# Kernel optimization log

Measured on AMD Instinct MI355X. Metric: run time of the kernel, lower is better.

## Reference

```python
import jax, jax.numpy as jnp
import numpy as np

B, C, L = 4, 512, 4096
H = 8
DH = C // H
MLP = 2048


def _ln(x, g, b, eps=1e-5):
    mu = x.mean(-1, keepdims=True)
    var = ((x - mu) ** 2).mean(-1, keepdims=True)
    return (x - mu) / jnp.sqrt(var + eps) * g + b


def setup_inputs() -> dict:
    key = jax.random.key(0)
    ks = jax.random.split(key, 16)
    s = 0.02
    d = {
        "x": jax.random.normal(ks[0], (B, C, L), jnp.float32),
        "Wq": jax.random.normal(ks[1], (C, C), jnp.float32) * s,
        "bq": jnp.zeros((C,), jnp.float32),
        "gq": jnp.ones((C,), jnp.float32),
        "betaq": jnp.zeros((C,), jnp.float32),
        "Wk": jax.random.normal(ks[2], (C, C), jnp.float32) * s,
        "bk": jnp.zeros((C,), jnp.float32),
        "gk": jnp.ones((C,), jnp.float32),
        "betak": jnp.zeros((C,), jnp.float32),
        "Wv": jax.random.normal(ks[3], (C, C), jnp.float32) * s,
        "bv": jnp.zeros((C,), jnp.float32),
        "gv": jnp.ones((C,), jnp.float32),
        "betav": jnp.zeros((C,), jnp.float32),
        "Wkq": jax.random.normal(ks[4], (C, C), jnp.float32) * s,
        "bkq": jnp.zeros((C,), jnp.float32),
        "Wkk": jax.random.normal(ks[5], (C, C), jnp.float32) * s,
        "bkk": jnp.zeros((C,), jnp.float32),
        "g_attn": jnp.ones((C,), jnp.float32),
        "b_attn": jnp.zeros((C,), jnp.float32),
        "W1": jax.random.normal(ks[6], (C, MLP), jnp.float32) * s,
        "b1": jnp.zeros((MLP,), jnp.float32),
        "W2": jax.random.normal(ks[7], (MLP, C), jnp.float32) * s,
        "b2": jnp.zeros((C,), jnp.float32),
    }
    return d


def _split_heads(t):
    # [B, L, C] -> [B, H, L, DH]
    b, l, _ = t.shape
    return t.reshape(b, l, H, DH).transpose(0, 2, 1, 3)


def reference(x, Wq, bq, gq, betaq, Wk, bk, gk, betak, Wv, bv, gv, betav,
              Wkq, bkq, Wkk, bkk, g_attn, b_attn, W1, b1, W2, b2):
    # x: [B, C, L] -> flatten(2).permute(0,2,1) -> [B, L, C]
    xf = jnp.transpose(x, (0, 2, 1))
    Q = _ln(xf @ Wq + bq, gq, betaq)            # [B, L, C]
    K = _ln(xf @ Wk + bk, gk, betak)            # [B, L, C]
    V = _ln(xf @ Wv + bv, gv, betav)            # [B, L, C]
    # add zero token to K, V (seq dim)
    z = jnp.zeros((x.shape[0], 1, C), x.dtype)
    K = jnp.concatenate([z, K], axis=1)         # [B, Lk, C], Lk = L+1
    V = jnp.concatenate([z, V], axis=1)
    phiQ = jnp.tanh(Q @ Wkq + bkq) + 1.0        # [B, L, C]
    phiK = jnp.tanh(K @ Wkk + bkk) + 1.0        # [B, Lk, C]

    Qh, Kh, Vh = _split_heads(Q), _split_heads(K), _split_heads(V)
    pQ, pK = _split_heads(phiQ), _split_heads(phiK)  # [B,H,L,DH], [B,H,Lk,DH]

    # softmax-reweighted phi_K: score from mean-query probe against K
    q_probe = Qh.mean(axis=2)                                   # [B,H,DH]
    score = jnp.einsum('bhd,bhld->bhl', q_probe, Kh) / jnp.sqrt(jnp.float32(DH))
    score = jax.nn.softmax(score, axis=-1)                      # [B,H,Lk]
    pKw = pK * score[..., None]                                 # [B,H,Lk,DH]

    kv = jnp.einsum('bhld,bhle->bhde', pKw, Vh)                 # [B,H,DH,DH]
    num = jnp.einsum('bhqd,bhde->bhqe', pQ, kv)                 # [B,H,L,DH]
    ksum = pKw.sum(axis=2)                                      # [B,H,DH]
    bottom = jnp.einsum('bhqd,bhd->bhq', pQ, ksum)[..., None] + 1e-6
    out_h = num / bottom                                        # [B,H,L,DH]

    out = out_h.transpose(0, 2, 1, 3).reshape(x.shape[0], -1, C)  # [B,L,C]
    a = _ln(out, g_attn, b_attn)
    m = jax.nn.gelu(a @ W1 + b1, approximate=False) @ W2 + b2
    res = a + m                                                 # residual MLP
    res = jnp.transpose(res, (0, 2, 1))                         # [B,C,L]
    return res + x
```

## Files before the change

### kernel.cpp

```cpp
#include <hip/hip_runtime.h>
#include <math.h>

#define B_ 4
#define C_ 512
#define L_ 4096
#define H_ 8
#define DH_ 64
#define MLP_ 2048
#define BL_ (B_*L_)
#define LK_ (L_+1)

typedef _Float16 f16;
typedef _Float16 f16x8 __attribute__((ext_vector_type(8)));
typedef _Float16 f16x4 __attribute__((ext_vector_type(4)));
typedef float f32x4 __attribute__((ext_vector_type(4)));

__device__ __forceinline__ void gl16(void* lds, const void* g) {
  __builtin_amdgcn_global_load_lds((const __attribute__((address_space(1))) void*)g,
                                   (__attribute__((address_space(3))) void*)lds,
                                   16, 0, 0);
}

__device__ __forceinline__ float frcp(float x) { return __builtin_amdgcn_rcpf(x); }

__global__ __launch_bounds__(256) void transpose_w5(const float* __restrict__ Wq,
                                                    const float* __restrict__ Wk,
                                                    const float* __restrict__ Wv,
                                                    const float* __restrict__ Wkq,
                                                    const float* __restrict__ Wkk,
                                                    f16* __restrict__ dst) {
  int z = blockIdx.z;
  const float* W = (z == 0) ? Wq : (z == 1) ? Wk : (z == 2) ? Wv : (z == 3) ? Wkq : Wkk;
  f16* Wt = dst + (size_t)z * C_ * C_;
  __shared__ float tile[32][33];
  int n0 = blockIdx.x * 32, k0 = blockIdx.y * 32;
  int tx = threadIdx.x & 31, ty = threadIdx.x >> 5;
#pragma unroll
  for (int i = 0; i < 4; ++i)
    tile[ty + i * 8][tx] = W[(size_t)(k0 + ty + i * 8) * C_ + n0 + tx];
  __syncthreads();
#pragma unroll
  for (int i = 0; i < 4; ++i)
    Wt[(size_t)(n0 + ty + i * 8) * C_ + k0 + tx] = (f16)tile[tx][ty + i * 8];
}

__global__ __launch_bounds__(256) void transpose_w(const float* __restrict__ W,
                                                   f16* __restrict__ Wt, int K, int N) {
  __shared__ float tile[32][33];
  int n0 = blockIdx.x * 32, k0 = blockIdx.y * 32;
  int tx = threadIdx.x & 31, ty = threadIdx.x >> 5;
#pragma unroll
  for (int i = 0; i < 4; ++i)
    tile[ty + i * 8][tx] = W[(size_t)(k0 + ty + i * 8) * N + n0 + tx];
  __syncthreads();
#pragma unroll
  for (int i = 0; i < 4; ++i)
    Wt[(size_t)(n0 + ty + i * 8) * K + k0 + tx] = (f16)tile[tx][ty + i * 8];
}

__global__ __launch_bounds__(256) void transpose_x(const float* __restrict__ x,
                                                   f16* __restrict__ xf) {
  __shared__ float tile[32][33];
  int b = blockIdx.z;
  int l0 = blockIdx.x * 32, c0 = blockIdx.y * 32;
  int tx = threadIdx.x & 31, ty = threadIdx.x >> 5;
#pragma unroll
  for (int i = 0; i < 4; ++i)
    tile[ty + i * 8][tx] = x[((size_t)b * C_ + c0 + ty + i * 8) * L_ + l0 + tx];
  __syncthreads();
#pragma unroll
  for (int i = 0; i < 4; ++i)
    xf[((size_t)b * L_ + l0 + ty + i * 8) * C_ + c0 + tx] = (f16)tile[tx][ty + i * 8];
}

__global__ __launch_bounds__(256) void pack_params(
    const float* bq, const float* bk, const float* bv,
    const float* gq, const float* gk, const float* gv,
    const float* betaq, const float* betak, const float* betav,
    const float* bkq, const float* bkk,
    float* bqkv, float* gqkv, float* betaqkv, float* bphi) {
  int i = blockIdx.x * 256 + threadIdx.x;
  int w = i >> 9, c = i & 511;
  bqkv[i]    = (w == 0 ? bq : (w == 1 ? bk : bv))[c];
  gqkv[i]    = (w == 0 ? gq : (w == 1 ? gk : gv))[c];
  betaqkv[i] = (w == 0 ? betaq : (w == 1 ? betak : betav))[c];
  if (i < 1024) bphi[i] = (i < 512) ? bkq[i] : bkk[i - 512];
}

template <int EPI>
__global__ __launch_bounds__(256, 2) void gemm64(const f16* __restrict__ A,
                                                 const f16* __restrict__ Bt,
                                                 const float* __restrict__ bias,
                                                 f16* __restrict__ Ch,
                                                 int N, int K,
                                                 const float* __restrict__ Bot,
                                                 const f16* __restrict__ Ares,
                                                 const float* __restrict__ Xres,
                                                 float* __restrict__ Fout,
                                                 long long zA, long long zB,
                                                 long long zC, long long zBias,
                                                 long long zBot) {
  __shared__ f16 smem[2 * 128 * 128];
  A  += (size_t)blockIdx.z * zA;
  Bt += (size_t)blockIdx.z * zB;
  if (EPI != 6) Ch += (size_t)blockIdx.z * zC;
  if (EPI == 3) Bot += (size_t)blockIdx.z * zBot;
  else          bias += (size_t)blockIdx.z * zBias;

  const int tid = threadIdx.x;
  const int lane = tid & 63, wv = tid >> 6;
  const int wm = wv >> 1, wn = wv & 1;
  const int bm = blockIdx.x * 128, bn = blockIdx.y * 128;
  const int l15 = lane & 15, q = lane >> 4;

  const int srow = tid >> 3;
  const int schunk = (tid & 7) ^ (srow & 7);
  const f16* pa = A + (size_t)(bm + srow) * K + schunk * 8;
  const f16* pb = Bt + (size_t)(bn + srow) * K + schunk * 8;
  f16* la = smem + tid * 8;
  f16* lb = smem + 8192 + tid * 8;
  const int sw0 = (q ^ (lane & 7)) * 8;
  const int sw1 = ((4 + q) ^ (lane & 7)) * 8;

  f32x4 acc[4][4] = {};

#pragma unroll
  for (int p = 0; p < 4; ++p) gl16(la + p * 2048, pa + (size_t)p * 32 * K);
#pragma unroll
  for (int p = 0; p < 4; ++p) gl16(lb + p * 2048, pb + (size_t)p * 32 * K);

  int cur = 0;
  for (int k0 = 0; k0 < K; k0 += 64) {
    __syncthreads();
    const int nxt = cur ^ 1;
    if (k0 + 64 < K) {
#pragma unroll
      for (int p = 0; p < 4; ++p) gl16(la + nxt * 16384 + p * 2048, pa + (size_t)p * 32 * K + k0 + 64);
#pragma unroll
      for (int p = 0; p < 4; ++p) gl16(lb + nxt * 16384 + p * 2048, pb + (size_t)p * 32 * K + k0 + 64);
    }
    const f16* As = smem + cur * 16384;
    const f16* Bs = As + 8192;
#pragma unroll
    for (int ks = 0; ks < 2; ++ks) {
      const int sw = ks ? sw1 : sw0;
      f16x8 af[4], bf[4];
#pragma unroll
      for (int i = 0; i < 4; ++i)
        af[i] = *(const f16x8*)&As[(wm * 64 + i * 16 + l15) * 64 + sw];
#pragma unroll
      for (int j = 0; j < 4; ++j)
        bf[j] = *(const f16x8*)&Bs[(wn * 64 + j * 16 + l15) * 64 + sw];
#pragma unroll
      for (int i = 0; i < 4; ++i)
#pragma unroll
        for (int j = 0; j < 4; ++j)
          acc[i][j] = __builtin_amdgcn_mfma_f32_16x16x32_f16(af[i], bf[j], acc[i][j], 0, 0, 0);
    }
    cur = nxt;
  }

  __syncthreads();
#pragma unroll
  for (int j = 0; j < 4; ++j) {
    int lc = wn * 64 + j * 16 + l15;
    float bb = (EPI == 3) ? 0.f : bias[bn + lc];
#pragma unroll
    for (int i = 0; i < 4; ++i) {
#pragma unroll
      for (int r = 0; r < 4; ++r) {
        int lr = wm * 64 + i * 16 + q * 4 + r;
        float v = acc[i][j][r] + bb;
        if (EPI == 1) {
          v = 2.0f * frcp(1.0f + __expf(-2.0f * v));
        } else if (EPI == 2) {
          v = v * frcp(1.0f + __expf(-1.5957691f * (v + 0.044715f * v * v * v)));
        } else if (EPI == 3) {
          v = v * frcp(Bot[(size_t)(bm + lr) * H_ + ((bn + lc) >> 6)] + 1e-6f);
        }
        smem[lr * 128 + ((((lc >> 3) ^ (lr & 15)) << 3) | (lc & 7))] = (f16)v;
      }
    }
  }
  __syncthreads();

  if (EPI != 6) {
#pragma unroll
    for (int p = 0; p < 8; ++p) {
      int idx = p * 256 + tid;
      int row = idx >> 4, ch = idx & 15;
      f16x8 vv = *(const f16x8*)&smem[row * 128 + ((ch ^ (row & 15)) << 3)];
      *(f16x8*)&Ch[(size_t)(bm + row) * N + bn + ch * 8] = vv;
    }
  } else {
#pragma unroll
    for (int p = 0; p < 8; ++p) {
      int idx = p * 256 + tid;
      int row = idx >> 4, ch = idx & 15;
      f16x8 av = *(const f16x8*)&Ares[(size_t)(bm + row) * C_ + bn + ch * 8];
      f16* sp = &smem[row * 128 + ((ch ^ (row & 15)) << 3)];
      f16x8 sv = *(const f16x8*)sp;
#pragma unroll
      for (int jj = 0; jj < 8; ++jj) sv[jj] = (f16)((float)sv[jj] + (float)av[jj]);
      *(f16x8*)sp = sv;
    }
    __syncthreads();
    int c = tid & 127, lh = tid >> 7;
    int b = bm >> 12, lbase = (bm & 4095) + lh * 64;
    const float* xp = Xres + ((size_t)b * C_ + bn + c) * L_ + lbase;
    float* op = Fout + ((size_t)b * C_ + bn + c) * L_ + lbase;
    int chi = c >> 3, clo = c & 7;
#pragma unroll
    for (int s = 0; s < 16; ++s) {
      int l = lh * 64 + s * 4;
      float4 xv = *(const float4*)(xp + s * 4);
      float4 r;
      r.x = (float)smem[(l + 0) * 128 + (((chi ^ ((l + 0) & 15)) << 3) | clo)] + xv.x;
      r.y = (float)smem[(l + 1) * 128 + (((chi ^ ((l + 1) & 15)) << 3) | clo)] + xv.y;
      r.z = (float)smem[(l + 2) * 128 + (((chi ^ ((l + 2) & 15)) << 3) | clo)] + xv.z;
      r.w = (float)smem[(l + 3) * 128 + (((chi ^ ((l + 3) & 15)) << 3) | clo)] + xv.w;
      *(float4*)(op + s * 4) = r;
    }
  }
}

__global__ __launch_bounds__(256) void ln16(const f16* __restrict__ X,
                                            const float* __restrict__ g,
                                            const float* __restrict__ bta,
                                            f16* __restrict__ Y, int threeway) {
  int wv = threadIdx.x >> 6, lane = threadIdx.x & 63;
  int r = blockIdx.x * 4 + wv;
  int token = r, which = 0;
  if (threeway) { token = r / 3; which = r - token * 3; }
  const f16* xr = X + (size_t)r * C_;
  f16x8 v = *(const f16x8*)(xr + lane * 8);
  float vals[8];
  float s = 0.f, s2 = 0.f;
#pragma unroll
  for (int j = 0; j < 8; ++j) { vals[j] = (float)v[j]; s += vals[j]; s2 += vals[j] * vals[j]; }
#pragma unroll
  for (int m_ = 1; m_ < 64; m_ <<= 1) { s += __shfl_xor(s, m_); s2 += __shfl_xor(s2, m_); }
  float mu = s * (1.f / C_);
  float var = s2 * (1.f / C_) - mu * mu;
  float rstd = rsqrtf(var + 1e-5f);
  const float* gp = g + which * C_;
  const float* bp = bta + which * C_;
  f16x8 o;
#pragma unroll
  for (int j = 0; j < 8; ++j) {
    int c = lane * 8 + j;
    o[j] = (f16)((vals[j] - mu) * rstd * gp[c] + bp[c]);
  }
  *(f16x8*)(Y + ((size_t)which * BL_ + token) * C_ + lane * 8) = o;
}

__global__ __launch_bounds__(256) void qprobe2(const f16* __restrict__ Q,
                                               float* __restrict__ qp) {
  int blk = blockIdx.x;
  int b = blk >> 6;
  int r0 = blk * 64;
  int t = threadIdx.x;
  int c8 = (t & 63) * 8, rg = t >> 6;
  float s[8] = {0.f, 0.f, 0.f, 0.f, 0.f, 0.f, 0.f, 0.f};
#pragma unroll
  for (int i = 0; i < 16; ++i) {
    const f16* row = Q + ((size_t)r0 + rg + i * 4) * C_ + c8;
    f16x8 v = *(const f16x8*)row;
#pragma unroll
    for (int j = 0; j < 8; ++j) s[j] += (float)v[j];
  }
  __shared__ float red[4][520];
#pragma unroll
  for (int j = 0; j < 8; ++j) red[rg][c8 + j] = s[j];
  __syncthreads();
  int c = t * 2;
  float a0 = red[0][c] + red[1][c] + red[2][c] + red[3][c];
  float a1 = red[0][c + 1] + red[1][c + 1] + red[2][c + 1] + red[3][c + 1];
  atomicAdd(&qp[b * C_ + c], a0);
  atomicAdd(&qp[b * C_ + c + 1], a1);
}

__global__ __launch_bounds__(256) void logits_kernel(const f16* __restrict__ Kh,
                                                     const float* __restrict__ qp,
                                                     float* __restrict__ score) {
  int wv = threadIdx.x >> 6, lane = threadIdx.x & 63;
  int token = blockIdx.x * 4 + wv;
  int b = token >> 12;
  int l = token & (L_ - 1);
  const f16* row = Kh + (size_t)token * C_;
  int h = lane >> 3, j0 = (lane & 7) * 8;
  const float* qph = qp + b * C_ + h * DH_ + j0;
  float p = 0.f;
#pragma unroll
  for (int j = 0; j < 8; ++j) p += qph[j] * (float)row[h * DH_ + j0 + j];
  p += __shfl_xor(p, 1); p += __shfl_xor(p, 2); p += __shfl_xor(p, 4);
  if ((lane & 7) == 0)
    score[((size_t)b * H_ + h) * LK_ + 1 + l] = p * (1.f / L_) * 0.125f;
}

__global__ __launch_bounds__(256) void softmax_kernel(float* __restrict__ score) {
  int bh = blockIdx.x, t = threadIdx.x;
  float* s = score + (size_t)bh * LK_;
  __shared__ float red[256];
  float mx = 0.f;
  for (int i = t; i < L_; i += 256) mx = fmaxf(mx, s[1 + i]);
  red[t] = mx; __syncthreads();
  for (int k = 128; k; k >>= 1) { if (t < k) red[t] = fmaxf(red[t], red[t + k]); __syncthreads(); }
  mx = red[0]; __syncthreads();
  float sum = (t == 0) ? expf(-mx) : 0.f;
  for (int i = t; i < L_; i += 256) { float e = expf(s[1 + i] - mx); s[1 + i] = e; sum += e; }
  red[t] = sum; __syncthreads();
  for (int k = 128; k; k >>= 1) { if (t < k) red[t] += red[t + k]; __syncthreads(); }
  float inv = 1.f / red[0];
  __syncthreads();
  for (int i = t; i < L_; i += 256) s[1 + i] *= inv;
  if (t == 0) s[0] = expf(-mx) * inv;
}

__global__ __launch_bounds__(256) void ksum_init(const float* __restrict__ score,
                                                 const float* __restrict__ bkk,
                                                 float* __restrict__ ksum) {
  int i = blockIdx.x * 256 + threadIdx.x;
  int bh = i >> 6, d = i & 63, h = bh & 7;
  float pk0 = tanhf(bkk[h * DH_ + d]) + 1.f;
  ksum[i] = score[(size_t)bh * LK_] * pk0;
}

#define PIDX(l, c) ((l) * 68 + (c))
#define AIDX(d, e) ((d) * 68 + (e) + ((((d) >> 3)) << 2))
__global__ __launch_bounds__(256, 2) void kv_part_kernel(const f16* __restrict__ phiK,
                                                         const f16* __restrict__ Vh,
                                                         const float* __restrict__ score,
                                                         float* __restrict__ kvp,
                                                         float* __restrict__ ksum) {
  __shared__ float sm0[4416];
  __shared__ float sm1[4416];
  int bh = blockIdx.y, b = bh >> 3, h = bh & 7;
  int part = blockIdx.x;
  int l0 = part * 256;
  int t = threadIdx.x, lane = t & 63, wv = t >> 6;
  int R = (lane >> 3) * 8, Cc = (lane & 7) * 8;
  float acc[8][8] = {};
  float ks[8] = {0.f, 0.f, 0.f, 0.f, 0.f, 0.f, 0.f, 0.f};

  for (int c = 0; c < 4; ++c) {
    int lc = l0 + c * 64;
    __syncthreads();
#pragma unroll
    for (int p = 0; p < 4; ++p) {
      int l = p * 16 + (t >> 4);
      int c4 = (t & 15) * 4;
      size_t grow = ((size_t)b * L_ + lc + l) * C_ + h * DH_ + c4;
      float w = score[(size_t)bh * LK_ + 1 + lc + l];
      f16x4 pk = *(const f16x4*)(phiK + grow);
      f16x4 vvv = *(const f16x4*)(Vh + grow);
      sm0[PIDX(l, c4) + 0] = w * (float)pk[0];
      sm0[PIDX(l, c4) + 1] = w * (float)pk[1];
      sm0[PIDX(l, c4) + 2] = w * (float)pk[2];
      sm0[PIDX(l, c4) + 3] = w * (float)pk[3];
      sm1[PIDX(l, c4) + 0] = (float)vvv[0];
      sm1[PIDX(l, c4) + 1] = (float)vvv[1];
      sm1[PIDX(l, c4) + 2] = (float)vvv[2];
      sm1[PIDX(l, c4) + 3] = (float)vvv[3];
    }
    __syncthreads();
#pragma unroll
    for (int i = 0; i < 16; ++i) {
      int ll = wv * 16 + i;
      float4 a0 = *(const float4*)&sm0[PIDX(ll, R)];
      float4 a1 = *(const float4*)&sm0[PIDX(ll, R + 4)];
      float4 b0 = *(const float4*)&sm1[PIDX(ll, Cc)];
      float4 b1 = *(const float4*)&sm1[PIDX(ll, Cc + 4)];
      float av[8] = {a0.x, a0.y, a0.z, a0.w, a1.x, a1.y, a1.z, a1.w};
      float bv2[8] = {b0.x, b0.y, b0.z, b0.w, b1.x, b1.y, b1.z, b1.w};
#pragma unroll
      for (int ii = 0; ii < 8; ++ii)
#pragma unroll
        for (int jj = 0; jj < 8; ++jj) acc[ii][jj] += av[ii] * bv2[jj];
      if ((lane & 7) == 0) {
#pragma unroll
        for (int ii = 0; ii < 8; ++ii) ks[ii] += av[ii];
      }
    }
  }

  __syncthreads();
  if ((lane & 7) == 0) {
#pragma unroll
    for (int i = 0; i < 8; ++i) sm1[wv * 64 + R + i] = ks[i];
  }
  for (int w = 0; w < 4; ++w) {
    if (wv == w) {
#pragma unroll
      for (int i = 0; i < 8; ++i) {
        float* p0 = &sm0[AIDX(R + i, Cc)];
        if (w == 0) {
          *(float4*)p0 = make_float4(acc[i][0], acc[i][1], acc[i][2], acc[i][3]);
          *(float4*)(p0 + 4) = make_float4(acc[i][4], acc[i][5], acc[i][6], acc[i][7]);
        } else {
          float4 o0 = *(const float4*)p0, o1 = *(const float4*)(p0 + 4);
          o0.x += acc[i][0]; o0.y += acc[i][1]; o0.z += acc[i][2]; o0.w += acc[i][3];
          o1.x += acc[i][4]; o1.y += acc[i][5]; o1.z += acc[i][6]; o1.w += acc[i][7];
          *(float4*)p0 = o0;
          *(float4*)(p0 + 4) = o1;
        }
      }
    }
    __syncthreads();
  }
  if (t < 64) {
    float s = sm1[t] + sm1[64 + t] + sm1[128 + t] + sm1[192 + t];
    atomicAdd(&ksum[bh * 64 + t], s);
  }
  float* dst = kvp + ((size_t)bh * 16 + part) * 4096;
#pragma unroll
  for (int i = 0; i < 16; ++i) {
    int idx = i * 256 + t;
    dst[idx] = sm0[AIDX(idx & 63, idx >> 6)];
  }
}

__global__ __launch_bounds__(256) void build_bd(const float* __restrict__ kvp,
                                                f16* __restrict__ BD) {
  size_t i = (size_t)blockIdx.x * 256 + threadIdx.x;
  int b = (int)(i >> 18);
  int nk = (int)(i & 262143);
  int n = nk >> 9, k = nk & 511;
  int hn = n >> 6, hk = k >> 6;
  float v = 0.f;
  if (hn == hk) {
    const float* p = kvp + ((size_t)(b * H_ + hn) * 16) * 4096 + (n & 63) * 64 + (k & 63);
#pragma unroll
    for (int pp = 0; pp < 16; ++pp) v += p[pp * 4096];
  }
  BD[i] = (f16)v;
}

__global__ __launch_bounds__(256) void bottom_kernel(const f16* __restrict__ phiQ,
                                                     const float* __restrict__ ksum,
                                                     float* __restrict__ bot) {
  int wv = threadIdx.x >> 6, lane = threadIdx.x & 63;
  int token = blockIdx.x * 4 + wv;
  int b = token >> 12;
  const f16* row = phiQ + (size_t)token * C_;
  int h = lane >> 3, j0 = (lane & 7) * 8;
  const float* ks = ksum + (b * H_ + h) * 64 + j0;
  float p = 0.f;
#pragma unroll
  for (int j = 0; j < 8; ++j) p += ks[j] * (float)row[h * DH_ + j0 + j];
  p += __shfl_xor(p, 1); p += __shfl_xor(p, 2); p += __shfl_xor(p, 4);
  if ((lane & 7) == 0) bot[(size_t)token * H_ + h] = p;
}

extern "C" void kernel_launch(void* const* d_in, const int* in_sizes, int n_in,
                              void* d_out, int out_size, void* d_ws, size_t ws_size,
                              hipStream_t stream) {
  (void)in_sizes; (void)n_in; (void)out_size; (void)ws_size;
  const float* x     = (const float*)d_in[0];
  const float* Wq    = (const float*)d_in[1];
  const float* bq    = (const float*)d_in[2];
  const float* gq    = (const float*)d_in[3];
  const float* betaq = (const float*)d_in[4];
  const float* Wk    = (const float*)d_in[5];
  const float* bk    = (const float*)d_in[6];
  const float* gk    = (const float*)d_in[7];
  const float* betak = (const float*)d_in[8];
  const float* Wv    = (const float*)d_in[9];
  const float* bv    = (const float*)d_in[10];
  const float* gv    = (const float*)d_in[11];
  const float* betav = (const float*)d_in[12];
  const float* Wkq   = (const float*)d_in[13];
  const float* bkq   = (const float*)d_in[14];
  const float* Wkk   = (const float*)d_in[15];
  const float* bkk   = (const float*)d_in[16];
  const float* g_at  = (const float*)d_in[17];
  const float* b_at  = (const float*)d_in[18];
  const float* W1    = (const float*)d_in[19];
  const float* b1    = (const float*)d_in[20];
  const float* W2    = (const float*)d_in[21];
  const float* b2    = (const float*)d_in[22];
  float* out = (float*)d_out;

  char* ws = (char*)d_ws;
  size_t off = 0;
  auto alloc = [&](size_t bytes) -> void* {
    void* p = ws + off;
    off += (bytes + 255) & ~(size_t)255;
    return p;
  };
  f16* U1    = (f16*)alloc((size_t)BL_ * MLP_ * 2);
  f16* QKVh  = (f16*)alloc((size_t)3 * BL_ * C_ * 2);
  f16* phiQK = (f16*)alloc((size_t)2 * BL_ * C_ * 2);
  f16* xf    = (f16*)alloc((size_t)BL_ * C_ * 2);
  f16* WqkvT = (f16*)alloc((size_t)3 * C_ * C_ * 2);
  f16* WkqT  = (f16*)alloc((size_t)C_ * C_ * 2);
  f16* WkkT  = (f16*)alloc((size_t)C_ * C_ * 2);
  f16* W1T   = (f16*)alloc((size_t)C_ * MLP_ * 2);
  f16* W2T   = (f16*)alloc((size_t)MLP_ * C_ * 2);
  f16* BD    = (f16*)alloc((size_t)B_ * C_ * C_ * 2);
  float* score = (float*)alloc((size_t)B_ * H_ * LK_ * 4);
  float* qp    = (float*)alloc((size_t)B_ * C_ * 4);
  float* kvp   = (float*)alloc((size_t)B_ * H_ * 16 * 4096 * 4);
  float* ksum  = (float*)alloc((size_t)B_ * H_ * DH_ * 4);
  float* bot   = (float*)alloc((size_t)BL_ * H_ * 4);
  float* bqkv    = (float*)alloc(1536 * 4);
  float* gqkv    = (float*)alloc(1536 * 4);
  float* betaqkv = (float*)alloc(1536 * 4);
  float* bphi    = (float*)alloc(1024 * 4);

  f16* tmpqkv = U1;
  f16* tmpA   = U1;
  f16* h1     = U1;
  f16* Qh = QKVh;
  f16* Kh = QKVh + (size_t)BL_ * C_;
  f16* Vh = QKVh + (size_t)2 * BL_ * C_;
  f16* ah = QKVh;
  f16* phiQ = phiQK;
  f16* phiK = phiQK + (size_t)BL_ * C_;

  dim3 blk(256);

  pack_params<<<6, blk, 0, stream>>>(bq, bk, bv, gq, gk, gv, betaq, betak, betav,
                                     bkq, bkk, bqkv, gqkv, betaqkv, bphi);

  transpose_w5<<<dim3(16, 16, 5), blk, 0, stream>>>(Wq, Wk, Wv, Wkq, Wkk, WqkvT);
  transpose_w<<<dim3(MLP_ / 32, C_ / 32), blk, 0, stream>>>(W1, W1T, C_, MLP_);
  transpose_w<<<dim3(C_ / 32, MLP_ / 32), blk, 0, stream>>>(W2, W2T, MLP_, C_);

  transpose_x<<<dim3(L_ / 32, C_ / 32, B_), blk, 0, stream>>>(x, xf);

  gemm64<5><<<dim3(BL_ / 128, 1536 / 128), blk, 0, stream>>>(
      xf, WqkvT, bqkv, tmpqkv, 1536, C_, nullptr, nullptr, nullptr, nullptr, 0, 0, 0, 0, 0);
  ln16<<<3 * BL_ / 4, blk, 0, stream>>>(tmpqkv, gqkv, betaqkv, QKVh, 1);

  hipMemsetAsync(qp, 0, (size_t)B_ * C_ * 4, stream);
  qprobe2<<<BL_ / 64, blk, 0, stream>>>(Qh, qp);

  gemm64<1><<<dim3(BL_ / 128, C_ / 128, 2), blk, 0, stream>>>(
      Qh, WkqT, bphi, phiQ, C_, C_, nullptr, nullptr, nullptr, nullptr,
      (long long)BL_ * C_, (long long)C_ * C_, (long long)BL_ * C_, (long long)C_, 0);

  logits_kernel<<<BL_ / 4, blk, 0, stream>>>(Kh, qp, score);
  softmax_kernel<<<B_ * H_, blk, 0, stream>>>(score);

  ksum_init<<<(B_ * H_ * DH_) / 256, blk, 0, stream>>>(score, bkk, ksum);
  kv_part_kernel<<<dim3(16, B_ * H_), blk, 0, stream>>>(phiK, Vh, score, kvp, ksum);

  build_bd<<<(B_ * C_ * C_) / 256, blk, 0, stream>>>(kvp, BD);
  bottom_kernel<<<BL_ / 4, blk, 0, stream>>>(phiQ, ksum, bot);

  gemm64<3><<<dim3(L_ / 128, C_ / 128, B_), blk, 0, stream>>>(
      phiQ, BD, nullptr, tmpA, C_, C_, bot, nullptr, nullptr, nullptr,
      (long long)L_ * C_, (long long)C_ * C_, (long long)L_ * C_, 0, (long long)L_ * H_);

  ln16<<<BL_ / 4, blk, 0, stream>>>(tmpA, g_at, b_at, ah, 0);

  gemm64<2><<<dim3(BL_ / 128, MLP_ / 128), blk, 0, stream>>>(
      ah, W1T, b1, h1, MLP_, C_, nullptr, nullptr, nullptr, nullptr, 0, 0, 0, 0, 0);
  gemm64<6><<<dim3(BL_ / 128, C_ / 128), blk, 0, stream>>>(
      h1, W2T, b2, nullptr, C_, MLP_, nullptr, ah, x, out, 0, 0, 0, 0, 0);
}
```

Before: 408.4 us.

## Fuse LayerNorm into full-row GEMM epilogues and merge small attention kernels

Adds a gemm_ln kernel that computes a full 128x512 output row block per workgroup (512 threads, 8 waves), so the LayerNorm statistics can be reduced in LDS and applied in the epilogue. This removes the separate ln16 passes and the fp16 round trip of the QKV projection and attention output. It also folds ksum_init into softmax and merges build_bd with bottom_kernel into a single launch. The trade-off is a larger per-block accumulator footprint (32 MFMA tiles per wave) and fewer blocks, which can lower occupancy and parallelism.

```diff
diff --git a/kernel.cpp b/kernel.cpp
--- a/kernel.cpp
+++ b/kernel.cpp
@@ -87,25 +87,162 @@
   if (i < 1024) bphi[i] = (i < 512) ? bkq[i] : bkk[i - 512];
 }
 
+template <int ATT>
+__global__ __launch_bounds__(512, 2) void gemm_ln(const f16* __restrict__ A,
+                                                  const f16* __restrict__ Bt,
+                                                  const float* __restrict__ bias,
+                                                  const float* __restrict__ g,
+                                                  const float* __restrict__ beta,
+                                                  const float* __restrict__ Bot,
+                                                  f16* __restrict__ Y) {
+  __shared__ f16 smem[40960];
+  __shared__ float sred[2][4][128];
+  __shared__ float smu[128], srs[128];
+  const int tid = threadIdx.x;
+  const int lane = tid & 63;
+  const int wv = tid >> 6;
+  const int wm = wv >> 2, wn = wv & 3;
+  const int l15 = lane & 15, q = lane >> 4;
+  const int bm = blockIdx.x * 128;
+  const int which = blockIdx.y;
+  const int zb = ATT ? (blockIdx.x >> 5) : which;
+  const f16* Bp = Bt + (size_t)zb * C_ * C_;
+  if (!ATT) Y += (size_t)which * BL_ * C_;
+
+  const int arow = tid >> 2;
+  const int ach = (tid & 3) ^ (arow & 3);
+  const f16* pa = A + (size_t)(bm + arow) * C_ + ach * 8;
+  const f16* pb = Bp + (size_t)arow * C_ + ach * 8;
+  const int sw = (q ^ (l15 & 3)) * 8;
+
+  f32x4 acc[4][8] = {};
+
+  gl16(smem + tid * 8, pa);
+#pragma unroll
+  for (int p = 0; p < 4; ++p)
+    gl16(smem + 4096 + p * 4096 + tid * 8, pb + (size_t)p * 128 * C_);
+
+  int cur = 0;
+  for (int k0 = 0; k0 < C_; k0 += 32) {
+    __syncthreads();
+    if (k0 + 32 < C_) {
+      int nb = (cur ^ 1) * 20480;
+      gl16(smem + nb + tid * 8, pa + k0 + 32);
+#pragma unroll
+      for (int p = 0; p < 4; ++p)
+        gl16(smem + nb + 4096 + p * 4096 + tid * 8, pb + (size_t)p * 128 * C_ + k0 + 32);
+    }
+    const f16* As = smem + cur * 20480;
+    const f16* Bs = As + 4096;
+    f16x8 af[4], bf[8];
+#pragma unroll
+    for (int i = 0; i < 4; ++i)
+      af[i] = *(const f16x8*)&As[(wm * 64 + i * 16 + l15) * 32 + sw];
+#pragma unroll
+    for (int j = 0; j < 8; ++j)
+      bf[j] = *(const f16x8*)&Bs[(wn * 128 + j * 16 + l15) * 32 + sw];
+#pragma unroll
+    for (int i = 0; i < 4; ++i)
+#pragma unroll
+      for (int j = 0; j < 8; ++j)
+        acc[i][j] = __builtin_amdgcn_mfma_f32_16x16x32_f16(af[i], bf[j], acc[i][j], 0, 0, 0);
+    cur ^= 1;
+  }
+
+  float bcol[8];
+#pragma unroll
+  for (int j = 0; j < 8; ++j)
+    bcol[j] = ATT ? 0.f : bias[which * C_ + wn * 128 + j * 16 + l15];
+
+#pragma unroll
+  for (int i = 0; i < 4; ++i) {
+#pragma unroll
+    for (int rv = 0; rv < 4; ++rv) {
+      int r = wm * 64 + i * 16 + q * 4 + rv;
+      float b0 = 1.f, b1 = 1.f;
+      if (ATT) {
+        b0 = frcp(Bot[(size_t)(bm + r) * H_ + wn * 2] + 1e-6f);
+        b1 = frcp(Bot[(size_t)(bm + r) * H_ + wn * 2 + 1] + 1e-6f);
+      }
+      float rs = 0.f, rq = 0.f;
+#pragma unroll
+      for (int j = 0; j < 8; ++j) {
+        float v = acc[i][j][rv] + bcol[j];
+        if (ATT) v *= (j < 4) ? b0 : b1;
+        acc[i][j][rv] = v;
+        rs += v; rq += v * v;
+      }
+#pragma unroll
+      for (int m_ = 1; m_ < 16; m_ <<= 1) { rs += __shfl_xor(rs, m_); rq += __shfl_xor(rq, m_); }
+      if (l15 == 0) { sred[0][wn][r] = rs; sred[1][wn][r] = rq; }
+    }
+  }
+  __syncthreads();
+  if (tid < 128) {
+    float s = sred[0][0][tid] + sred[0][1][tid] + sred[0][2][tid] + sred[0][3][tid];
+    float sq = sred[1][0][tid] + sred[1][1][tid] + sred[1][2][tid] + sred[1][3][tid];
+    float mu = s * (1.f / C_);
+    float var = sq * (1.f / C_) - mu * mu;
+    smu[tid] = mu;
+    srs[tid] = rsqrtf(var + 1e-5f);
+  }
+  __syncthreads();
+
+  float gcol[8], btc[8];
+#pragma unroll
+  for (int j = 0; j < 8; ++j) {
+    int col = wn * 128 + j * 16 + l15;
+    gcol[j] = g[(ATT ? 0 : which * C_) + col];
+    btc[j] = beta[(ATT ? 0 : which * C_) + col];
+  }
+
+#pragma unroll
+  for (int hc = 0; hc < 2; ++hc) {
+    if (wm == hc) {
+#pragma unroll
+      for (int i = 0; i < 4; ++i) {
+#pragma unroll
+        for (int rv = 0; rv < 4; ++rv) {
+          int r = wm * 64 + i * 16 + q * 4 + rv;
+          float mu = smu[r], rstd = srs[r];
+          int lr = r - hc * 64;
+#pragma unroll
+          for (int j = 0; j < 8; ++j) {
+            int col = wn * 128 + j * 16 + l15;
+            float v = (acc[i][j][rv] - mu) * rstd * gcol[j] + btc[j];
+            smem[lr * 524 + col] = (f16)v;
+          }
+        }
+      }
+    }
+    __syncthreads();
+#pragma unroll
+    for (int p = 0; p < 8; ++p) {
+      int idx = p * 512 + tid;
+      int r = idx >> 6, cc = idx & 63;
+      f16x8 o = *(const f16x8*)&smem[r * 524 + cc * 8];
+      *(f16x8*)&Y[(size_t)(bm + hc * 64 + r) * C_ + cc * 8] = o;
+    }
+    __syncthreads();
+  }
+}
+
 template <int EPI>
 __global__ __launch_bounds__(256, 2) void gemm64(const f16* __restrict__ A,
                                                  const f16* __restrict__ Bt,
                                                  const float* __restrict__ bias,
                                                  f16* __restrict__ Ch,
                                                  int N, int K,
-                                                 const float* __restrict__ Bot,
                                                  const f16* __restrict__ Ares,
                                                  const float* __restrict__ Xres,
                                                  float* __restrict__ Fout,
                                                  long long zA, long long zB,
-                                                 long long zC, long long zBias,
-                                                 long long zBot) {
+                                                 long long zC, long long zBias) {
   __shared__ f16 smem[2 * 128 * 128];
   A  += (size_t)blockIdx.z * zA;
   Bt += (size_t)blockIdx.z * zB;
   if (EPI != 6) Ch += (size_t)blockIdx.z * zC;
-  if (EPI == 3) Bot += (size_t)blockIdx.z * zBot;
-  else          bias += (size_t)blockIdx.z * zBias;
+  bias += (size_t)blockIdx.z * zBias;
 
   const int tid = threadIdx.x;
   const int lane = tid & 63, wv = tid >> 6;
@@ -164,7 +301,7 @@
 #pragma unroll
   for (int j = 0; j < 4; ++j) {
     int lc = wn * 64 + j * 16 + l15;
-    float bb = (EPI == 3) ? 0.f : bias[bn + lc];
+    float bb = bias[bn + lc];
 #pragma unroll
     for (int i = 0; i < 4; ++i) {
 #pragma unroll
@@ -175,8 +312,6 @@
           v = 2.0f * frcp(1.0f + __expf(-2.0f * v));
         } else if (EPI == 2) {
           v = v * frcp(1.0f + __expf(-1.5957691f * (v + 0.044715f * v * v * v)));
-        } else if (EPI == 3) {
-          v = v * frcp(Bot[(size_t)(bm + lr) * H_ + ((bn + lc) >> 6)] + 1e-6f);
         }
         smem[lr * 128 + ((((lc >> 3) ^ (lr & 15)) << 3) | (lc & 7))] = (f16)v;
       }
@@ -222,36 +357,6 @@
       *(float4*)(op + s * 4) = r;
     }
   }
-}
-
-__global__ __launch_bounds__(256) void ln16(const f16* __restrict__ X,
-                                            const float* __restrict__ g,
-                                            const float* __restrict__ bta,
-                                            f16* __restrict__ Y, int threeway) {
-  int wv = threadIdx.x >> 6, lane = threadIdx.x & 63;
-  int r = blockIdx.x * 4 + wv;
-  int token = r, which = 0;
-  if (threeway) { token = r / 3; which = r - token * 3; }
-  const f16* xr = X + (size_t)r * C_;
-  f16x8 v = *(const f16x8*)(xr + lane * 8);
-  float vals[8];
-  float s = 0.f, s2 = 0.f;
-#pragma unroll
-  for (int j = 0; j < 8; ++j) { vals[j] = (float)v[j]; s += vals[j]; s2 += vals[j] * vals[j]; }
-#pragma unroll
-  for (int m_ = 1; m_ < 64; m_ <<= 1) { s += __shfl_xor(s, m_); s2 += __shfl_xor(s2, m_); }
-  float mu = s * (1.f / C_);
-  float var = s2 * (1.f / C_) - mu * mu;
-  float rstd = rsqrtf(var + 1e-5f);
-  const float* gp = g + which * C_;
-  const float* bp = bta + which * C_;
-  f16x8 o;
-#pragma unroll
-  for (int j = 0; j < 8; ++j) {
-    int c = lane * 8 + j;
-    o[j] = (f16)((vals[j] - mu) * rstd * gp[c] + bp[c]);
-  }
-  *(f16x8*)(Y + ((size_t)which * BL_ + token) * C_ + lane * 8) = o;
 }
 
 __global__ __launch_bounds__(256) void qprobe2(const f16* __restrict__ Q,
@@ -298,7 +403,9 @@
     score[((size_t)b * H_ + h) * LK_ + 1 + l] = p * (1.f / L_) * 0.125f;
 }
 
-__global__ __launch_bounds__(256) void softmax_kernel(float* __restrict__ score) {
+__global__ __launch_bounds__(256) void softmax_kernel(float* __restrict__ score,
+                                                      const float* __restrict__ bkk,
+                                                      float* __restrict__ ksum) {
   int bh = blockIdx.x, t = threadIdx.x;
   float* s = score + (size_t)bh * LK_;
   __shared__ float red[256];
@@ -314,16 +421,12 @@
   float inv = 1.f / red[0];
   __syncthreads();
   for (int i = t; i < L_; i += 256) s[1 + i] *= inv;
-  if (t == 0) s[0] = expf(-mx) * inv;
-}
-
-__global__ __launch_bounds__(256) void ksum_init(const float* __restrict__ score,
-                                                 const float* __restrict__ bkk,
-                                                 float* __restrict__ ksum) {
-  int i = blockIdx.x * 256 + threadIdx.x;
-  int bh = i >> 6, d = i & 63, h = bh & 7;
-  float pk0 = tanhf(bkk[h * DH_ + d]) + 1.f;
-  ksum[i] = score[(size_t)bh * LK_] * pk0;
+  float s0 = expf(-mx) * inv;
+  if (t == 0) s[0] = s0;
+  if (t < 64) {
+    int h = bh & 7;
+    ksum[bh * 64 + t] = s0 * (tanhf(bkk[h * DH_ + t]) + 1.f);
+  }
 }
 
 #define PIDX(l, c) ((l) * 68 + (c))
@@ -420,36 +523,37 @@
   }
 }
 
-__global__ __launch_bounds__(256) void build_bd(const float* __restrict__ kvp,
-                                                f16* __restrict__ BD) {
-  size_t i = (size_t)blockIdx.x * 256 + threadIdx.x;
-  int b = (int)(i >> 18);
-  int nk = (int)(i & 262143);
-  int n = nk >> 9, k = nk & 511;
-  int hn = n >> 6, hk = k >> 6;
-  float v = 0.f;
-  if (hn == hk) {
-    const float* p = kvp + ((size_t)(b * H_ + hn) * 16) * 4096 + (n & 63) * 64 + (k & 63);
-#pragma unroll
-    for (int pp = 0; pp < 16; ++pp) v += p[pp * 4096];
-  }
-  BD[i] = (f16)v;
-}
-
-__global__ __launch_bounds__(256) void bottom_kernel(const f16* __restrict__ phiQ,
-                                                     const float* __restrict__ ksum,
-                                                     float* __restrict__ bot) {
-  int wv = threadIdx.x >> 6, lane = threadIdx.x & 63;
-  int token = blockIdx.x * 4 + wv;
-  int b = token >> 12;
-  const f16* row = phiQ + (size_t)token * C_;
-  int h = lane >> 3, j0 = (lane & 7) * 8;
-  const float* ks = ksum + (b * H_ + h) * 64 + j0;
-  float p = 0.f;
-#pragma unroll
-  for (int j = 0; j < 8; ++j) p += ks[j] * (float)row[h * DH_ + j0 + j];
-  p += __shfl_xor(p, 1); p += __shfl_xor(p, 2); p += __shfl_xor(p, 4);
-  if ((lane & 7) == 0) bot[(size_t)token * H_ + h] = p;
+__global__ __launch_bounds__(256) void bd_bottom(const float* __restrict__ kvp,
+                                                 f16* __restrict__ BD,
+                                                 const f16* __restrict__ phiQ,
+                                                 const float* __restrict__ ksum,
+                                                 float* __restrict__ bot) {
+  if (blockIdx.x < 4096) {
+    size_t i = (size_t)blockIdx.x * 256 + threadIdx.x;
+    int b = (int)(i >> 18);
+    int nk = (int)(i & 262143);
+    int n = nk >> 9, k = nk & 511;
+    int hn = n >> 6, hk = k >> 6;
+    float v = 0.f;
+    if (hn == hk) {
+      const float* p = kvp + ((size_t)(b * H_ + hn) * 16) * 4096 + (n & 63) * 64 + (k & 63);
+#pragma unroll
+      for (int pp = 0; pp < 16; ++pp) v += p[pp * 4096];
+    }
+    BD[i] = (f16)v;
+  } else {
+    int wv = threadIdx.x >> 6, lane = threadIdx.x & 63;
+    int token = (blockIdx.x - 4096) * 4 + wv;
+    int b = token >> 12;
+    const f16* row = phiQ + (size_t)token * C_;
+    int h = lane >> 3, j0 = (lane & 7) * 8;
+    const float* ks = ksum + (b * H_ + h) * 64 + j0;
+    float p = 0.f;
+#pragma unroll
+    for (int j = 0; j < 8; ++j) p += ks[j] * (float)row[h * DH_ + j0 + j];
+    p += __shfl_xor(p, 1); p += __shfl_xor(p, 2); p += __shfl_xor(p, 4);
+    if ((lane & 7) == 0) bot[(size_t)token * H_ + h] = p;
+  }
 }
 
 extern "C" void kernel_launch(void* const* d_in, const int* in_sizes, int n_in,
@@ -488,7 +592,7 @@
     off += (bytes + 255) & ~(size_t)255;
     return p;
   };
-  f16* U1    = (f16*)alloc((size_t)BL_ * MLP_ * 2);
+  f16* h1    = (f16*)alloc((size_t)BL_ * MLP_ * 2);
   f16* QKVh  = (f16*)alloc((size_t)3 * BL_ * C_ * 2);
   f16* phiQK = (f16*)alloc((size_t)2 * BL_ * C_ * 2);
   f16* xf    = (f16*)alloc((size_t)BL_ * C_ * 2);
@@ -508,9 +612,6 @@
   float* betaqkv = (float*)alloc(1536 * 4);
   float* bphi    = (float*)alloc(1024 * 4);
 
-  f16* tmpqkv = U1;
-  f16* tmpA   = U1;
-  f16* h1     = U1;
   f16* Qh = QKVh;
   f16* Kh = QKVh + (size_t)BL_ * C_;
   f16* Vh = QKVh + (size_t)2 * BL_ * C_;
@@ -526,37 +627,29 @@
   transpose_w5<<<dim3(16, 16, 5), blk, 0, stream>>>(Wq, Wk, Wv, Wkq, Wkk, WqkvT);
   transpose_w<<<dim3(MLP_ / 32, C_ / 32), blk, 0, stream>>>(W1, W1T, C_, MLP_);
   transpose_w<<<dim3(C_ / 32, MLP_ / 32), blk, 0, stream>>>(W2, W2T, MLP_, C_);
-
   transpose_x<<<dim3(L_ / 32, C_ / 32, B_), blk, 0, stream>>>(x, xf);
 
-  gemm64<5><<<dim3(BL_ / 128, 1536 / 128), blk, 0, stream>>>(
-      xf, WqkvT, bqkv, tmpqkv, 1536, C_, nullptr, nullptr, nullptr, nullptr, 0, 0, 0, 0, 0);
-  ln16<<<3 * BL_ / 4, blk, 0, stream>>>(tmpqkv, gqkv, betaqkv, QKVh, 1);
+  gemm_ln<0><<<dim3(BL_ / 128, 3), dim3(512), 0, stream>>>(
+      xf, WqkvT, bqkv, gqkv, betaqkv, nullptr, QKVh);
 
   hipMemsetAsync(qp, 0, (size_t)B_ * C_ * 4, stream);
   qprobe2<<<BL_ / 64, blk, 0, stream>>>(Qh, qp);
 
   gemm64<1><<<dim3(BL_ / 128, C_ / 128, 2), blk, 0, stream>>>(
-      Qh, WkqT, bphi, phiQ, C_, C_, nullptr, nullptr, nullptr, nullptr,
-      (long long)BL_ * C_, (long long)C_ * C_, (long long)BL_ * C_, (long long)C_, 0);
+      Qh, WkqT, bphi, phiQ, C_, C_, nullptr, nullptr, nullptr,
+      (long long)BL_ * C_, (long long)C_ * C_, (long long)BL_ * C_, (long long)C_);
 
   logits_kernel<<<BL_ / 4, blk, 0, stream>>>(Kh, qp, score);
-  softmax_kernel<<<B_ * H_, blk, 0, stream>>>(score);
-
-  ksum_init<<<(B_ * H_ * DH_) / 256, blk, 0, stream>>>(score, bkk, ksum);
+  softmax_kernel<<<B_ * H_, blk, 0, stream>>>(score, bkk, ksum);
+
   kv_part_kernel<<<dim3(16, B_ * H_), blk, 0, stream>>>(phiK, Vh, score, kvp, ksum);
-
-  build_bd<<<(B_ * C_ * C_) / 256, blk, 0, stream>>>(kvp, BD);
-  bottom_kernel<<<BL_ / 4, blk, 0, stream>>>(phiQ, ksum, bot);
-
-  gemm64<3><<<dim3(L_ / 128, C_ / 128, B_), blk, 0, stream>>>(
-      phiQ, BD, nullptr, tmpA, C_, C_, bot, nullptr, nullptr, nullptr,
-      (long long)L_ * C_, (long long)C_ * C_, (long long)L_ * C_, 0, (long long)L_ * H_);
-
-  ln16<<<BL_ / 4, blk, 0, stream>>>(tmpA, g_at, b_at, ah, 0);
+  bd_bottom<<<8192, blk, 0, stream>>>(kvp, BD, phiQ, ksum, bot);
+
+  gemm_ln<1><<<dim3(BL_ / 128, 1), dim3(512), 0, stream>>>(
+      phiQ, BD, nullptr, g_at, b_at, bot, ah);
 
   gemm64<2><<<dim3(BL_ / 128, MLP_ / 128), blk, 0, stream>>>(
-      ah, W1T, b1, h1, MLP_, C_, nullptr, nullptr, nullptr, nullptr, 0, 0, 0, 0, 0);
+      ah, W1T, b1, h1, MLP_, C_, nullptr, nullptr, nullptr, 0, 0, 0, 0);
   gemm64<6><<<dim3(BL_ / 128, C_ / 128), blk, 0, stream>>>(
-      h1, W2T, b2, nullptr, C_, MLP_, nullptr, ah, x, out, 0, 0, 0, 0, 0);
-}
+      h1, W2T, b2, nullptr, C_, MLP_, ah, x, out, 0, 0, 0, 0);
+}
```

Result: no change. 411.6 us (+0.8%).
